# Kernel optimization log

Hardware: AMD Instinct MI355X
Metric: run time of the kernel (lower is better)

The kernel has to match this reference:

```python
import jax, jax.numpy as jnp
import numpy as np

VOCAB, EMB, HID = 32000, 256, 512
B, S = 16, 256


def setup_inputs() -> dict:
    key = jax.random.key(0)
    ks = jax.random.split(key, 7)
    x = jax.random.randint(ks[0], (B, S), 0, VOCAB, dtype=jnp.int32)
    E = jax.random.normal(ks[1], (VOCAB, EMB), dtype=jnp.float32) * 0.02
    # GRUCell kernels, gate order [z, r, h], reset_after=True (keras default)
    W = jax.random.normal(ks[2], (EMB, 3 * HID), dtype=jnp.float32) * 0.02
    U = jax.random.normal(ks[3], (HID, 3 * HID), dtype=jnp.float32) * 0.02
    b = jnp.zeros((2, 3 * HID), dtype=jnp.float32)  # [input_bias, recurrent_bias]
    Wd = jax.random.normal(ks[4], (HID, VOCAB), dtype=jnp.float32) * 0.02
    bd = jnp.zeros((VOCAB,), dtype=jnp.float32)
    return {"x": x, "E": E, "W": W, "U": U, "b": b, "Wd": Wd, "bd": bd}


def _gru_sequence(emb, W, U, b):
    # emb: [B, S, EMB]. Precompute all input-side gate projections at once.
    xw = jnp.einsum('bse,eh->bsh', emb, W) + b[0]          # [B, S, 3H]
    xw_t = jnp.transpose(xw, (1, 0, 2))                     # [S, B, 3H]
    b_rec = b[1]
    H = U.shape[0]

    def step(h, xt):
        rec = h @ U + b_rec                                 # [B, 3H]
        xz, xr, xh = xt[:, :H], xt[:, H:2 * H], xt[:, 2 * H:]
        rz, rr, rh = rec[:, :H], rec[:, H:2 * H], rec[:, 2 * H:]
        z = jax.nn.sigmoid(xz + rz)
        r = jax.nn.sigmoid(xr + rr)
        hh = jnp.tanh(xh + r * rh)                          # reset_after=True form
        h_new = z * h + (1.0 - z) * hh
        return h_new, h_new

    h0 = jnp.zeros((emb.shape[0], H), dtype=emb.dtype)
    _, hs = jax.lax.scan(step, h0, xw_t)                    # hs: [S, B, H]
    return jnp.transpose(hs, (1, 0, 2))                     # [B, S, H]


def reference(x, E, W, U, b, Wd, bd):
    emb = E[x]                                              # [B, S, EMB]
    h = _gru_sequence(emb, W, U, b)                         # [B, S, H]
    logits = jnp.einsum('bsh,hv->bsv', h, Wd) + bd          # [B, S, VOCAB]
    return logits
```

## Files before the change

### kernel.cpp

```cpp
#include <hip/hip_runtime.h>
#include <hip/hip_bf16.h>
#include <stdint.h>
#include <stddef.h>

#define NB 16
#define NS 256
#define NH 512
#define NE 256
#define NV 32000
#define NM (NB*NS)
#define N3H 1536

typedef __attribute__((ext_vector_type(8))) short short8v;
typedef __attribute__((ext_vector_type(4))) float float4v;
typedef __attribute__((address_space(1))) const unsigned int gas_u32;
typedef __attribute__((address_space(3))) unsigned int las_u32;

static __device__ __forceinline__ unsigned short f2bf(float f) {
  __hip_bfloat16 h = __float2bfloat16(f);
  return *reinterpret_cast<unsigned short*>(&h);
}
static __device__ __forceinline__ float bf2f(unsigned short u) {
  union { unsigned int u; float f; } c;
  c.u = ((unsigned int)u) << 16;
  return c.f;
}
static __device__ __forceinline__ float fast_tanh(float x) {
  float t = __expf(2.f * x);
  return (t - 1.f) / (t + 1.f);
}

__global__ void gather_emb(const int* __restrict__ x, const float* __restrict__ E,
                           unsigned short* __restrict__ A) {
  int m = blockIdx.x * 4 + (threadIdx.x >> 6);
  int lane = threadIdx.x & 63;
  int t = x[m];
  float4 v = reinterpret_cast<const float4*>(E + (size_t)t * NE)[lane];
  ushort4 o = make_ushort4(f2bf(v.x), f2bf(v.y), f2bf(v.z), f2bf(v.w));
  reinterpret_cast<ushort4*>(A + (size_t)m * NE)[lane] = o;
}

template<typename T>
__global__ void transpose_conv(const float* __restrict__ in, T* __restrict__ out,
                               int R, int C) {
  __shared__ float tile[32][33];
  int c0 = blockIdx.x * 32, r0 = blockIdx.y * 32;
  int tx = threadIdx.x, ty = threadIdx.y;
  #pragma unroll
  for (int i = 0; i < 32; i += 8)
    tile[ty + i][tx] = in[(size_t)(r0 + ty + i) * C + (c0 + tx)];
  __syncthreads();
  #pragma unroll
  for (int i = 0; i < 32; i += 8) {
    float v = tile[tx][ty + i];
    if constexpr (sizeof(T) == 2)
      out[(size_t)(c0 + ty + i) * R + (r0 + tx)] = (T)f2bf(v);
    else
      out[(size_t)(c0 + ty + i) * R + (r0 + tx)] = (T)v;
  }
}

template<bool OUT_BF16>
__launch_bounds__(256)
__global__ void gemm_bt(const unsigned short* __restrict__ A,
                        const unsigned short* __restrict__ BT,
                        const float* __restrict__ bias,
                        void* __restrict__ out, int N, int K) {
  __shared__ unsigned short As[128 * 32];
  __shared__ unsigned short Bs[128 * 32];
  const int tid = threadIdx.x;
  const int lane = tid & 63, wave = tid >> 6;
  const int wr = wave >> 1, wc = wave & 1;
  int nwg = gridDim.x * gridDim.y;
  int bid0 = blockIdx.y * gridDim.x + blockIdx.x;
  int q = nwg >> 3, r8 = nwg & 7;
  int xcd = bid0 & 7, idx = bid0 >> 3;
  int bid = (xcd < r8 ? xcd * (q + 1) : r8 * (q + 1) + (xcd - r8) * q) + idx;
  const int m0 = (bid / gridDim.x) * 128, n0 = (bid % gridDim.x) * 128;
  const int lr = lane & 15, lg = lane >> 4;
  float4v acc[4][4] = {};

  for (int k0 = 0; k0 < K; k0 += 32) {
    #pragma unroll
    for (int qq = 0; qq < 2; ++qq) {
      int byteoff = qq * 4096 + tid * 16;
      int rr = byteoff >> 6, cb = byteoff & 63;
      const char* ga = (const char*)A + ((size_t)(m0 + rr) * K + k0) * 2 + cb;
      const char* gb = (const char*)BT + ((size_t)(n0 + rr) * K + k0) * 2 + cb;
      char* la = (char*)As + qq * 4096 + wave * 1024;
      char* lb = (char*)Bs + qq * 4096 + wave * 1024;
      __builtin_amdgcn_global_load_lds((gas_u32*)ga, (las_u32*)la, 16, 0, 0);
      __builtin_amdgcn_global_load_lds((gas_u32*)gb, (las_u32*)lb, 16, 0, 0);
    }
    __syncthreads();
    short8v a[4], b[4];
    #pragma unroll
    for (int i = 0; i < 4; ++i)
      a[i] = *(const short8v*)((const char*)As + (wr * 64 + i * 16 + lr) * 64 + lg * 16);
    #pragma unroll
    for (int j = 0; j < 4; ++j)
      b[j] = *(const short8v*)((const char*)Bs + (wc * 64 + j * 16 + lr) * 64 + lg * 16);
    #pragma unroll
    for (int i = 0; i < 4; ++i) {
      #pragma unroll
      for (int j = 0; j < 4; ++j)
        acc[i][j] = __builtin_amdgcn_mfma_f32_16x16x32_bf16(a[i], b[j], acc[i][j], 0, 0, 0);
    }
    __syncthreads();
  }
  #pragma unroll
  for (int i = 0; i < 4; ++i) {
    int row = m0 + wr * 64 + i * 16 + lg * 4;
    #pragma unroll
    for (int j = 0; j < 4; ++j) {
      int col = n0 + wc * 64 + j * 16 + lr;
      float bv = bias[col];
      #pragma unroll
      for (int rr = 0; rr < 4; ++rr) {
        float v = acc[i][j][rr] + bv;
        if constexpr (OUT_BF16)
          ((unsigned short*)out)[(size_t)(row + rr) * N + col] = f2bf(v);
        else
          ((float*)out)[(size_t)(row + rr) * N + col] = v;
      }
    }
  }
}

#define SENT 0xFFFFFFFFu
__launch_bounds__(256, 1)
__global__ void gru_kernel(const unsigned short* __restrict__ xw,
                           const float* __restrict__ UT,
                           const float* __restrict__ bvec,
                           unsigned int* __restrict__ Hex) {
  const int blk = blockIdx.x, tid = threadIdx.x;
  const int grp = blk >> 4, wq = blk & 15;
  const int lane = tid & 63, w = tid >> 6;
  const int lr = lane & 15, lg = lane >> 4;
  __shared__ __align__(16) unsigned short h_lds[2][4 * 512];
  __shared__ __align__(16) float scratch[4][96];

  const int D0 = 32 * wq;
  short8v Bf0[16], Bf1[16];
  {
    int dloc = D0 + 8 * w + (lr & 7);
    int colg0 = (lr < 8) ? dloc : (512 + dloc);
    const float* u0 = UT + (size_t)colg0 * 512 + lg * 8;
    const float* u1 = UT + (size_t)(1024 + dloc) * 512 + lg * 8;
    #pragma unroll
    for (int kk = 0; kk < 16; ++kk) {
      float4 a0 = *(const float4*)(u0 + kk * 32);
      float4 a1 = *(const float4*)(u0 + kk * 32 + 4);
      float4 c0 = *(const float4*)(u1 + kk * 32);
      float4 c1 = *(const float4*)(u1 + kk * 32 + 4);
      short8v t0, t1;
      t0[0] = (short)f2bf(a0.x); t0[1] = (short)f2bf(a0.y);
      t0[2] = (short)f2bf(a0.z); t0[3] = (short)f2bf(a0.w);
      t0[4] = (short)f2bf(a1.x); t0[5] = (short)f2bf(a1.y);
      t0[6] = (short)f2bf(a1.z); t0[7] = (short)f2bf(a1.w);
      t1[0] = (short)f2bf(c0.x); t1[1] = (short)f2bf(c0.y);
      t1[2] = (short)f2bf(c0.z); t1[3] = (short)f2bf(c0.w);
      t1[4] = (short)f2bf(c1.x); t1[5] = (short)f2bf(c1.y);
      t1[6] = (short)f2bf(c1.z); t1[7] = (short)f2bf(c1.w);
      Bf0[kk] = t0; Bf1[kk] = t1;
    }
  }
  for (int i = tid; i < 512; i += 256)
    reinterpret_cast<uint4*>(h_lds)[i] = make_uint4(0, 0, 0, 0);

  const int b = lane & 3, di = lane >> 2;
  const int d = D0 + 8 * w + di;
  const int hi = di & 1;
  float h_old = 0.f, bz = 0.f, br = 0.f, bh = 0.f;
  const unsigned int* xp = nullptr;
  if (lane < 32) {
    const float* brec = bvec + 1536;
    bz = brec[d]; br = brec[512 + d]; bh = brec[1024 + d];
    xp = (const unsigned int*)xw + (size_t)(grp * 4 + b) * 256 * 768 + ((d & ~1) >> 1);
  }
  const bool own = ((tid >> 2) & 15) == wq;
  const int pbb = tid >> 6;
  __syncthreads();

  int p = 0;
  for (int s = 0; s < 256; ++s) {
    unsigned int xzw = 0, xrw = 0, xhw = 0;
    if (lane < 32) { xzw = xp[0]; xrw = xp[256]; xhw = xp[512]; xp += 768; }

    if (s > 0 && !own) {
      const unsigned long long* src =
          (const unsigned long long*)(Hex + ((size_t)s * 4 + grp) * 1024 + tid * 4);
      unsigned long long v0 = __hip_atomic_load(&src[0], __ATOMIC_RELAXED, __HIP_MEMORY_SCOPE_AGENT);
      unsigned long long v1 = __hip_atomic_load(&src[1], __ATOMIC_RELAXED, __HIP_MEMORY_SCOPE_AGENT);
      unsigned int pend = 3;
      char* dst = (char*)h_lds[p];
      int dpp = (tid & 63) * 4;
      while (pend) {
        unsigned int np = 0;
        if (pend & 1) {
          if ((unsigned int)v0 != SENT && (unsigned int)(v0 >> 32) != SENT)
            *(unsigned long long*)(dst + ((pbb * 1024 + dpp * 4) ^ (pbb << 4))) = v0;
          else np |= 1;
        }
        if (pend & 2) {
          if ((unsigned int)v1 != SENT && (unsigned int)(v1 >> 32) != SENT)
            *(unsigned long long*)(dst + ((pbb * 1024 + (dpp + 2) * 4) ^ (pbb << 4))) = v1;
          else np |= 2;
        }
        pend = np;
        if (pend) {
          __builtin_amdgcn_s_sleep(1);
          if (pend & 1) v0 = __hip_atomic_load(&src[0], __ATOMIC_RELAXED, __HIP_MEMORY_SCOPE_AGENT);
          if (pend & 2) v1 = __hip_atomic_load(&src[1], __ATOMIC_RELAXED, __HIP_MEMORY_SCOPE_AGENT);
        }
      }
    }
    __syncthreads();

    float4v acc0 = {}, acc1 = {};
    const char* hb = (const char*)h_lds[p];
    #pragma unroll
    for (int kk = 0; kk < 16; ++kk) {
      int off = ((lane & 3) * 1024 + kk * 64 + lg * 16) ^ ((lane & 3) << 4);
      short8v a = *(const short8v*)(hb + off);
      acc0 = __builtin_amdgcn_mfma_f32_16x16x32_bf16(a, Bf0[kk], acc0, 0, 0, 0);
      acc1 = __builtin_amdgcn_mfma_f32_16x16x32_bf16(a, Bf1[kk], acc1, 0, 0, 0);
    }
    if (lg == 0) {
      *(float4*)&scratch[w][lr * 4] = *(float4*)&acc0;
      if (lr < 8)
        *(float4*)&scratch[w][64 + lr * 4] = *(float4*)&acc1;
    }
    if (lane < 32) {
      float rz = scratch[w][lane];
      float rr = scratch[w][32 + lane];
      float rh = scratch[w][64 + lane];
      float xz = bf2f((unsigned short)(hi ? (xzw >> 16) : (xzw & 0xffff)));
      float xr = bf2f((unsigned short)(hi ? (xrw >> 16) : (xrw & 0xffff)));
      float xh = bf2f((unsigned short)(hi ? (xhw >> 16) : (xhw & 0xffff)));
      float z = 1.f / (1.f + __expf(-(xz + rz + bz)));
      float r = 1.f / (1.f + __expf(-(xr + rr + br)));
      float hh = fast_tanh(xh + r * (rh + bh));
      h_old = z * h_old + (1.f - z) * hh;
      unsigned int mine = f2bf(h_old);
      unsigned int part = (unsigned int)__shfl_xor((int)mine, 4);
      if ((lane & 4) == 0) {
        unsigned int pack = mine | (part << 16);
        int wordi = b * 256 + wq * 16 + w * 4 + (di >> 1);
        __hip_atomic_store(&Hex[(size_t)(s + 1) * 4096 + grp * 1024 + wordi], pack,
                           __ATOMIC_RELAXED, __HIP_MEMORY_SCOPE_AGENT);
        *(unsigned int*)((char*)h_lds[p ^ 1] +
                         ((b * 1024 + (wordi & 255) * 4) ^ (b << 4))) = pack;
      }
    }
    p ^= 1;
  }
}

__launch_bounds__(256)
__global__ void dec_gemm(const char* __restrict__ HexB,
                         const unsigned short* __restrict__ WdT,
                         const float* __restrict__ bd,
                         float* __restrict__ out) {
  __shared__ unsigned short As[128 * 32];
  __shared__ unsigned short Bs[128 * 32];
  const int tid = threadIdx.x;
  const int lane = tid & 63, wave = tid >> 6;
  const int wr = wave >> 1, wc = wave & 1;
  const int lr = lane & 15, lg = lane >> 4;
  int bid0 = blockIdx.x;
  int bid = (bid0 & 7) * 1000 + (bid0 >> 3);
  const int mt = bid & 31, nt = bid >> 5;
  const int b = mt >> 1, s0 = (mt & 1) * 128;
  const int n0 = nt * 128;
  float4v acc[4][4] = {};

  for (int k0 = 0; k0 < NH; k0 += 32) {
    #pragma unroll
    for (int qq = 0; qq < 2; ++qq) {
      int off = qq * 4096 + tid * 16;
      int rloc = off >> 6, cb = off & 63;
      int s = s0 + rloc;
      const char* ga = HexB + ((size_t)(s + 1) * 4 + (b >> 2)) * 4096 +
                       (size_t)(b & 3) * 1024 + k0 * 2 + cb;
      const char* gb = (const char*)WdT + ((size_t)(n0 + rloc) * 512 + k0) * 2 + cb;
      __builtin_amdgcn_global_load_lds((gas_u32*)ga,
          (las_u32*)((char*)As + qq * 4096 + wave * 1024), 16, 0, 0);
      __builtin_amdgcn_global_load_lds((gas_u32*)gb,
          (las_u32*)((char*)Bs + qq * 4096 + wave * 1024), 16, 0, 0);
    }
    __syncthreads();
    short8v a[4], bb[4];
    #pragma unroll
    for (int i = 0; i < 4; ++i)
      a[i] = *(const short8v*)((const char*)As + (wr * 64 + i * 16 + lr) * 64 + lg * 16);
    #pragma unroll
    for (int j = 0; j < 4; ++j)
      bb[j] = *(const short8v*)((const char*)Bs + (wc * 64 + j * 16 + lr) * 64 + lg * 16);
    #pragma unroll
    for (int i = 0; i < 4; ++i) {
      #pragma unroll
      for (int j = 0; j < 4; ++j)
        acc[i][j] = __builtin_amdgcn_mfma_f32_16x16x32_bf16(a[i], bb[j], acc[i][j], 0, 0, 0);
    }
    __syncthreads();
  }
  #pragma unroll
  for (int i = 0; i < 4; ++i) {
    int l = wr * 64 + i * 16 + lg * 4;
    #pragma unroll
    for (int j = 0; j < 4; ++j) {
      int col = n0 + wc * 64 + j * 16 + lr;
      float bv = bd[col];
      #pragma unroll
      for (int rr = 0; rr < 4; ++rr) {
        size_t m = (size_t)(b * 256 + s0 + l + rr);
        __builtin_nontemporal_store(acc[i][j][rr] + bv, &out[m * NV + col]);
      }
    }
  }
}

extern "C" void kernel_launch(void* const* d_in, const int* in_sizes, int n_in,
                              void* d_out, int out_size, void* d_ws, size_t ws_size,
                              hipStream_t stream) {
  const int*   x  = (const int*)d_in[0];
  const float* E  = (const float*)d_in[1];
  const float* W  = (const float*)d_in[2];
  const float* U  = (const float*)d_in[3];
  const float* bv = (const float*)d_in[4];
  const float* Wd = (const float*)d_in[5];
  const float* bd = (const float*)d_in[6];
  float* out = (float*)d_out;

  char* ws = (char*)d_ws;
  size_t off = 0;
  auto alloc = [&](size_t bytes) -> void* {
    void* p = ws + off;
    off = (off + bytes + 255) & ~(size_t)255;
    return p;
  };
  unsigned short* Aemb = (unsigned short*)alloc((size_t)NM * NE * 2);
  unsigned short* WT   = (unsigned short*)alloc((size_t)N3H * NE * 2);
  float*          UT   = (float*)alloc((size_t)N3H * NH * 4);
  unsigned short* xwb  = (unsigned short*)alloc((size_t)NM * N3H * 2);
  unsigned short* WdT  = (unsigned short*)alloc((size_t)NV * NH * 2);
  unsigned int*   Hex  = (unsigned int*)alloc((size_t)257 * 4096 * 4);

  hipMemsetAsync(Hex, 0xFF, (size_t)257 * 4096 * 4, stream);

  gather_emb<<<NM / 4, 256, 0, stream>>>(x, E, Aemb);
  transpose_conv<unsigned short><<<dim3(N3H / 32, NE / 32), dim3(32, 8), 0, stream>>>(W,  WT,  NE, N3H);
  transpose_conv<float>         <<<dim3(N3H / 32, NH / 32), dim3(32, 8), 0, stream>>>(U,  UT,  NH, N3H);
  transpose_conv<unsigned short><<<dim3(NV / 32,  NH / 32), dim3(32, 8), 0, stream>>>(Wd, WdT, NH, NV);

  gemm_bt<true><<<dim3(N3H / 128, NM / 128), 256, 0, stream>>>(Aemb, WT, bv, xwb, N3H, NE);

  gru_kernel<<<64, 256, 0, stream>>>(xwb, UT, bv, Hex);

  dec_gemm<<<8000, 256, 0, stream>>>((const char*)Hex, WdT, bd, out);
}
```

Measured before the change: 688.1 us.

## Repartition GRU recurrence to 2 batches per group with 8 blocks each

The persistent GRU kernel changes its work split from 4 batch rows per group over 16 blocks to 2 batch rows per group over 8 blocks. Each wave now owns 16 hidden units across all three gates, held as three MFMA B-fragment sets, instead of 8 units split across two MFMAs. This shrinks the set of blocks that must exchange hidden state each step and lets each thread poll a single 64-bit word, cutting cross-block synchronisation latency per timestep. The cost is more register-resident weights per wave and less useful MFMA row occupancy, since only 2 of 16 A rows carry data. The Hex layout and the decoder GEMM's address calculation are updated to match.

```diff
diff --git a/kernel.cpp b/kernel.cpp
--- a/kernel.cpp
+++ b/kernel.cpp
@@ -134,52 +134,43 @@
                            const float* __restrict__ bvec,
                            unsigned int* __restrict__ Hex) {
   const int blk = blockIdx.x, tid = threadIdx.x;
-  const int grp = blk >> 4, wq = blk & 15;
+  const int grp = blk >> 3, wq = blk & 7;
   const int lane = tid & 63, w = tid >> 6;
-  const int lr = lane & 15, lg = lane >> 4;
-  __shared__ __align__(16) unsigned short h_lds[2][4 * 512];
+  const int lg = lane >> 4, lr = lane & 15;
+  __shared__ __align__(16) unsigned short h_lds[2][1024];
   __shared__ __align__(16) float scratch[4][96];
 
-  const int D0 = 32 * wq;
-  short8v Bf0[16], Bf1[16];
-  {
-    int dloc = D0 + 8 * w + (lr & 7);
-    int colg0 = (lr < 8) ? dloc : (512 + dloc);
-    const float* u0 = UT + (size_t)colg0 * 512 + lg * 8;
-    const float* u1 = UT + (size_t)(1024 + dloc) * 512 + lg * 8;
+  const int D0w = 64 * wq + 16 * w;
+  short8v Bf[3][16];
+  #pragma unroll
+  for (int c = 0; c < 3; ++c) {
+    const float* up = UT + (size_t)(c * 512 + D0w + lr) * 512 + lg * 8;
     #pragma unroll
     for (int kk = 0; kk < 16; ++kk) {
-      float4 a0 = *(const float4*)(u0 + kk * 32);
-      float4 a1 = *(const float4*)(u0 + kk * 32 + 4);
-      float4 c0 = *(const float4*)(u1 + kk * 32);
-      float4 c1 = *(const float4*)(u1 + kk * 32 + 4);
-      short8v t0, t1;
-      t0[0] = (short)f2bf(a0.x); t0[1] = (short)f2bf(a0.y);
-      t0[2] = (short)f2bf(a0.z); t0[3] = (short)f2bf(a0.w);
-      t0[4] = (short)f2bf(a1.x); t0[5] = (short)f2bf(a1.y);
-      t0[6] = (short)f2bf(a1.z); t0[7] = (short)f2bf(a1.w);
-      t1[0] = (short)f2bf(c0.x); t1[1] = (short)f2bf(c0.y);
-      t1[2] = (short)f2bf(c0.z); t1[3] = (short)f2bf(c0.w);
-      t1[4] = (short)f2bf(c1.x); t1[5] = (short)f2bf(c1.y);
-      t1[6] = (short)f2bf(c1.z); t1[7] = (short)f2bf(c1.w);
-      Bf0[kk] = t0; Bf1[kk] = t1;
-    }
-  }
-  for (int i = tid; i < 512; i += 256)
-    reinterpret_cast<uint4*>(h_lds)[i] = make_uint4(0, 0, 0, 0);
-
-  const int b = lane & 3, di = lane >> 2;
-  const int d = D0 + 8 * w + di;
-  const int hi = di & 1;
+      float4 v0 = *(const float4*)(up + kk * 32);
+      float4 v1 = *(const float4*)(up + kk * 32 + 4);
+      short8v t;
+      t[0] = (short)f2bf(v0.x); t[1] = (short)f2bf(v0.y);
+      t[2] = (short)f2bf(v0.z); t[3] = (short)f2bf(v0.w);
+      t[4] = (short)f2bf(v1.x); t[5] = (short)f2bf(v1.y);
+      t[6] = (short)f2bf(v1.z); t[7] = (short)f2bf(v1.w);
+      Bf[c][kk] = t;
+    }
+  }
+  reinterpret_cast<uint4*>(h_lds)[tid] = make_uint4(0, 0, 0, 0);
+
+  const int b = lane & 1, di = lane >> 1;
+  const int d = D0w + di, hi = d & 1;
   float h_old = 0.f, bz = 0.f, br = 0.f, bh = 0.f;
   const unsigned int* xp = nullptr;
   if (lane < 32) {
     const float* brec = bvec + 1536;
     bz = brec[d]; br = brec[512 + d]; bh = brec[1024 + d];
-    xp = (const unsigned int*)xw + (size_t)(grp * 4 + b) * 256 * 768 + ((d & ~1) >> 1);
-  }
-  const bool own = ((tid >> 2) & 15) == wq;
-  const int pbb = tid >> 6;
+    xp = (const unsigned int*)xw + (size_t)(grp * 2 + b) * 256 * 768 + (d >> 1);
+  }
+  const bool own = ((tid >> 4) & 7) == wq;
+  const int pbb = tid >> 7;
+  const int pm  = (2 * tid) & 255;
   __syncthreads();
 
   int p = 0;
@@ -189,52 +180,35 @@
 
     if (s > 0 && !own) {
       const unsigned long long* src =
-          (const unsigned long long*)(Hex + ((size_t)s * 4 + grp) * 1024 + tid * 4);
-      unsigned long long v0 = __hip_atomic_load(&src[0], __ATOMIC_RELAXED, __HIP_MEMORY_SCOPE_AGENT);
-      unsigned long long v1 = __hip_atomic_load(&src[1], __ATOMIC_RELAXED, __HIP_MEMORY_SCOPE_AGENT);
-      unsigned int pend = 3;
-      char* dst = (char*)h_lds[p];
-      int dpp = (tid & 63) * 4;
-      while (pend) {
-        unsigned int np = 0;
-        if (pend & 1) {
-          if ((unsigned int)v0 != SENT && (unsigned int)(v0 >> 32) != SENT)
-            *(unsigned long long*)(dst + ((pbb * 1024 + dpp * 4) ^ (pbb << 4))) = v0;
-          else np |= 1;
-        }
-        if (pend & 2) {
-          if ((unsigned int)v1 != SENT && (unsigned int)(v1 >> 32) != SENT)
-            *(unsigned long long*)(dst + ((pbb * 1024 + (dpp + 2) * 4) ^ (pbb << 4))) = v1;
-          else np |= 2;
-        }
-        pend = np;
-        if (pend) {
-          __builtin_amdgcn_s_sleep(1);
-          if (pend & 1) v0 = __hip_atomic_load(&src[0], __ATOMIC_RELAXED, __HIP_MEMORY_SCOPE_AGENT);
-          if (pend & 2) v1 = __hip_atomic_load(&src[1], __ATOMIC_RELAXED, __HIP_MEMORY_SCOPE_AGENT);
-        }
+          (const unsigned long long*)(Hex + (size_t)s * 4096 + grp * 512 + 2 * tid);
+      unsigned long long v = __hip_atomic_load(src, __ATOMIC_RELAXED, __HIP_MEMORY_SCOPE_AGENT);
+      while ((unsigned int)v == SENT || (unsigned int)(v >> 32) == SENT) {
+        __builtin_amdgcn_s_sleep(1);
+        v = __hip_atomic_load(src, __ATOMIC_RELAXED, __HIP_MEMORY_SCOPE_AGENT);
       }
-    }
-    __syncthreads();
-
-    float4v acc0 = {}, acc1 = {};
+      *(unsigned long long*)((char*)h_lds[p] + ((pbb * 1024 + pm * 4) ^ (pbb << 4))) = v;
+    }
+    __syncthreads();
+
+    float4v a0 = {}, a1 = {}, a2 = {};
     const char* hb = (const char*)h_lds[p];
     #pragma unroll
     for (int kk = 0; kk < 16; ++kk) {
-      int off = ((lane & 3) * 1024 + kk * 64 + lg * 16) ^ ((lane & 3) << 4);
+      int off = ((lane & 1) * 1024 + kk * 64 + lg * 16) ^ ((lane & 1) << 4);
       short8v a = *(const short8v*)(hb + off);
-      acc0 = __builtin_amdgcn_mfma_f32_16x16x32_bf16(a, Bf0[kk], acc0, 0, 0, 0);
-      acc1 = __builtin_amdgcn_mfma_f32_16x16x32_bf16(a, Bf1[kk], acc1, 0, 0, 0);
+      a0 = __builtin_amdgcn_mfma_f32_16x16x32_bf16(a, Bf[0][kk], a0, 0, 0, 0);
+      a1 = __builtin_amdgcn_mfma_f32_16x16x32_bf16(a, Bf[1][kk], a1, 0, 0, 0);
+      a2 = __builtin_amdgcn_mfma_f32_16x16x32_bf16(a, Bf[2][kk], a2, 0, 0, 0);
     }
     if (lg == 0) {
-      *(float4*)&scratch[w][lr * 4] = *(float4*)&acc0;
-      if (lr < 8)
-        *(float4*)&scratch[w][64 + lr * 4] = *(float4*)&acc1;
+      *(float2*)&scratch[w][lr * 2]      = make_float2(a0[0], a0[1]);
+      *(float2*)&scratch[w][32 + lr * 2] = make_float2(a1[0], a1[1]);
+      *(float2*)&scratch[w][64 + lr * 2] = make_float2(a2[0], a2[1]);
     }
     if (lane < 32) {
-      float rz = scratch[w][lane];
-      float rr = scratch[w][32 + lane];
-      float rh = scratch[w][64 + lane];
+      float rz = scratch[w][di * 2 + b];
+      float rr = scratch[w][32 + di * 2 + b];
+      float rh = scratch[w][64 + di * 2 + b];
       float xz = bf2f((unsigned short)(hi ? (xzw >> 16) : (xzw & 0xffff)));
       float xr = bf2f((unsigned short)(hi ? (xrw >> 16) : (xrw & 0xffff)));
       float xh = bf2f((unsigned short)(hi ? (xhw >> 16) : (xhw & 0xffff)));
@@ -243,14 +217,15 @@
       float hh = fast_tanh(xh + r * (rh + bh));
       h_old = z * h_old + (1.f - z) * hh;
       unsigned int mine = f2bf(h_old);
-      unsigned int part = (unsigned int)__shfl_xor((int)mine, 4);
-      if ((lane & 4) == 0) {
-        unsigned int pack = mine | (part << 16);
-        int wordi = b * 256 + wq * 16 + w * 4 + (di >> 1);
-        __hip_atomic_store(&Hex[(size_t)(s + 1) * 4096 + grp * 1024 + wordi], pack,
-                           __ATOMIC_RELAXED, __HIP_MEMORY_SCOPE_AGENT);
-        *(unsigned int*)((char*)h_lds[p ^ 1] +
-                         ((b * 1024 + (wordi & 255) * 4) ^ (b << 4))) = pack;
+      unsigned int pack = mine | ((unsigned int)__shfl_xor((int)mine, 2) << 16);
+      unsigned int hip2 = (unsigned int)__shfl_xor((int)pack, 4);
+      if ((lane & 6) == 0) {
+        unsigned long long u = (unsigned long long)pack | ((unsigned long long)hip2 << 32);
+        int m = 32 * wq + 8 * w + 2 * (lane >> 3);
+        __hip_atomic_store((unsigned long long*)&Hex[(size_t)(s + 1) * 4096 + grp * 512 +
+                                                     b * 256 + m],
+                           u, __ATOMIC_RELAXED, __HIP_MEMORY_SCOPE_AGENT);
+        *(unsigned long long*)((char*)h_lds[p ^ 1] + ((b * 1024 + m * 4) ^ (b << 4))) = u;
       }
     }
     p ^= 1;
@@ -281,8 +256,8 @@
       int off = qq * 4096 + tid * 16;
       int rloc = off >> 6, cb = off & 63;
       int s = s0 + rloc;
-      const char* ga = HexB + ((size_t)(s + 1) * 4 + (b >> 2)) * 4096 +
-                       (size_t)(b & 3) * 1024 + k0 * 2 + cb;
+      const char* ga = HexB + ((size_t)(s + 1) * 4096 + (b >> 1) * 512 + (b & 1) * 256) * 4
+                       + k0 * 2 + cb;
       const char* gb = (const char*)WdT + ((size_t)(n0 + rloc) * 512 + k0) * 2 + cb;
       __builtin_amdgcn_global_load_lds((gas_u32*)ga,
           (las_u32*)((char*)As + qq * 4096 + wave * 1024), 16, 0, 0);
```

New measurement: 672.2 us. 2.3% less time.
